# Optimization experiments

Hardware: AMD Instinct MI355X
Metric: run time of the kernel (lower is better)

The kernel has to match this reference:

```python
import jax, jax.numpy as jnp
import numpy as np

N_NODES = 50000
N_EDGES = 800000


def _gcn_norm(edge_index, n_nodes):
    # add self loops, compute symmetric normalization coefficients (PyG GCNConv)
    loop = jnp.arange(n_nodes, dtype=edge_index.dtype)
    src = jnp.concatenate([edge_index[0], loop])
    dst = jnp.concatenate([edge_index[1], loop])
    deg = jax.ops.segment_sum(jnp.ones_like(dst, dtype=jnp.float32), dst, num_segments=n_nodes)
    dinv = jnp.where(deg > 0, jax.lax.rsqrt(deg), 0.0)
    coef = dinv[src] * dinv[dst]  # [E + N]
    return src, dst, coef


def _gcn_conv(x, src, dst, coef, W, b, n_nodes):
    h = x @ W                                   # [N, out]
    msg = h[src] * coef[:, None]                # gather + scale
    agg = jax.ops.segment_sum(msg, dst, num_segments=n_nodes)
    return agg + b


def setup_inputs() -> dict:
    key = jax.random.key(0)
    ks = jax.random.split(key, 10)
    d_in, d_hid, d_out = 128, 512, 256
    num_class = [30, 25, 20, 3000]
    inp = {
        "x": jax.random.normal(ks[0], (N_NODES, d_in), dtype=jnp.float32),
        "edge_index": jax.random.randint(ks[1], (2, N_EDGES), 0, N_NODES, dtype=jnp.int64),
        "W1": jax.random.normal(ks[2], (d_in, d_hid), dtype=jnp.float32) / np.sqrt(d_in),
        "b1": jnp.zeros((d_hid,), dtype=jnp.float32),
        "W2": jax.random.normal(ks[3], (d_hid, d_out), dtype=jnp.float32) / np.sqrt(d_hid),
        "b2": jnp.zeros((d_out,), dtype=jnp.float32),
        "Wt": jax.random.normal(ks[4], (d_out, num_class[0]), dtype=jnp.float32) / np.sqrt(d_out),
        "bt": jnp.zeros((num_class[0],), dtype=jnp.float32),
        "Ws": jax.random.normal(ks[5], (d_out, num_class[1]), dtype=jnp.float32) / np.sqrt(d_out),
        "bs": jnp.zeros((num_class[1],), dtype=jnp.float32),
        "Wf": jax.random.normal(ks[6], (d_out, num_class[2]), dtype=jnp.float32) / np.sqrt(d_out),
        "bf": jnp.zeros((num_class[2],), dtype=jnp.float32),
        "Wa": jax.random.normal(ks[7], (d_out, num_class[3]), dtype=jnp.float32) / np.sqrt(d_out),
        "ba": jnp.zeros((num_class[3],), dtype=jnp.float32),
    }
    return inp


def reference(x, edge_index, W1, b1, W2, b2, Wt, bt, Ws, bs, Wf, bf, Wa, ba):
    n = x.shape[0]
    src, dst, coef = _gcn_norm(edge_index, n)
    h = jax.nn.relu(_gcn_conv(x, src, dst, coef, W1, b1, n))
    # dropout is identity at eval time
    g = _gcn_conv(h, src, dst, coef, W2, b2, n)  # graph embedding [N, 256]
    out_type = g @ Wt + bt
    out_school = g @ Ws + bs
    out_time = g @ Wf + bf
    out_author = g @ Wa + ba
    return (out_type, out_school, out_time, out_author)
```

## Files before the change

kernel.cpp:

```cpp
#include <hip/hip_runtime.h>

#define N_NODES 50000
#define N_EDGES 800000

typedef __attribute__((ext_vector_type(8))) short short8;
typedef __attribute__((ext_vector_type(4))) float f32x4;
typedef __attribute__((ext_vector_type(4))) unsigned short u16x4;

__device__ inline unsigned short f2b(float f) {
  union { float f; unsigned int u; } c; c.f = f;
  unsigned int u = c.u;
  u += 0x7FFF + ((u >> 16) & 1);
  return (unsigned short)(u >> 16);
}
__device__ inline float b2f_lo(unsigned int u) {
  union { unsigned int u; float f; } c; c.u = u << 16; return c.f;
}
__device__ inline float b2f_hi(unsigned int u) {
  union { unsigned int u; float f; } c; c.u = u & 0xFFFF0000u; return c.f;
}


__global__ void k_deg(const int* __restrict__ ei, int* __restrict__ deg) {
  int e = blockIdx.x * 256 + threadIdx.x;
  if (e < N_EDGES) atomicAdd(&deg[ei[N_EDGES + e]], 1);
}

__global__ void k_scan(const int* __restrict__ cnt, int* __restrict__ rowptr,
                       float* __restrict__ dinv) {
  __shared__ int wsum[16];
  int tid = threadIdx.x, lane = tid & 63, wv = tid >> 6;
  int carry = 0;
  for (int base = 0; base < N_NODES; base += 1024) {
    int i = base + tid;
    int v = (i < N_NODES) ? cnt[i] : 0;
    if (i < N_NODES) dinv[i] = rsqrtf((float)(v + 1));
    int s = v;
#pragma unroll
    for (int off = 1; off < 64; off <<= 1) {
      int u = __shfl_up(s, off, 64);
      if (lane >= off) s += u;
    }
    if (lane == 63) wsum[wv] = s;
    __syncthreads();
    int ws = (lane < 16) ? wsum[lane] : 0;
#pragma unroll
    for (int off = 1; off < 16; off <<= 1) {
      int u = __shfl_up(ws, off, 64);
      if (lane >= off && lane < 16) ws += u;
    }
    int wOff = (wv == 0) ? 0 : __shfl(ws, wv - 1, 64);
    int total = __shfl(ws, 15, 64);
    if (i < N_NODES) rowptr[i] = carry + wOff + (s - v);
    carry += total;
    __syncthreads();
  }
  if (tid == 0) rowptr[N_NODES] = carry;
}

__global__ void k_fill(const int* __restrict__ ei, const int* __restrict__ rowptr,
                       int* __restrict__ cur, int* __restrict__ csr) {
  int e = blockIdx.x * 256 + threadIdx.x;
  if (e < N_EDGES) {
    int d = ei[N_EDGES + e];
    int p = atomicAdd(&cur[d], 1);
    csr[rowptr[d] + p] = ei[e];
  }
}


#define CVT_UNITS (N_NODES * 128 / 4)
#define PW1_UNITS (4 * 4 * 512)
#define PW2_UNITS (2 * 16 * 512)
#define PH_UNITS  102400

__global__ void k_prep(const float* __restrict__ x, unsigned short* __restrict__ xb,
                       const float* __restrict__ W1, unsigned short* __restrict__ Bp0,
                       const float* __restrict__ W2, unsigned short* __restrict__ Bp1,
                       const float* __restrict__ Wt, const float* __restrict__ Ws,
                       const float* __restrict__ Wf, const float* __restrict__ Wa,
                       const float* __restrict__ bt, const float* __restrict__ bs,
                       const float* __restrict__ bfv, const float* __restrict__ ba,
                       unsigned short* __restrict__ BpH, float* __restrict__ bcat) {
  int idx = blockIdx.x * 256 + threadIdx.x;
  if (idx < CVT_UNITS) {
    float4 v = ((const float4*)x)[idx];
    ushort4 o; o.x = f2b(v.x); o.y = f2b(v.y); o.z = f2b(v.z); o.w = f2b(v.w);
    ((ushort4*)xb)[idx] = o;
    return;
  }
  idx -= CVT_UNITS;
  if (idx < PW1_UNITS) {
    const int KS = 4, N = 512;
    int grp = idx & 3, col = (idx >> 2) & 127;
    int rest = idx >> 9;
    int s = rest % KS, chunk = rest / KS;
    int gcol = chunk * 128 + col, k0 = s * 32 + grp * 8;
    unsigned short o[8];
#pragma unroll
    for (int j = 0; j < 8; ++j) o[j] = f2b(W1[(size_t)(k0 + j) * N + gcol]);
    *(short8*)(Bp0 + (size_t)idx * 8) = *(short8*)o;
    return;
  }
  idx -= PW1_UNITS;
  if (idx < PW2_UNITS) {
    const int KS = 16, N = 256;
    int grp = idx & 3, col = (idx >> 2) & 127;
    int rest = idx >> 9;
    int s = rest % KS, chunk = rest / KS;
    int gcol = chunk * 128 + col, k0 = s * 32 + grp * 8;
    unsigned short o[8];
#pragma unroll
    for (int j = 0; j < 8; ++j) o[j] = f2b(W2[(size_t)(k0 + j) * N + gcol]);
    *(short8*)(Bp1 + (size_t)idx * 8) = *(short8*)o;
    return;
  }
  idx -= PW2_UNITS;
  if (idx < PH_UNITS) {
    const int KS = 8;
    int grp = idx & 3, col = (idx >> 2) & 127;
    int rest = idx >> 9;
    int s = rest % KS, chunk = rest / KS;
    int gcol = chunk * 128 + col, k0 = s * 32 + grp * 8;
    const float* W = Wt; int ld = 30, c = 0;
    bool ok = true;
    if (gcol < 30)                        { W = Wt; ld = 30;   c = gcol; }
    else if (gcol < 55)                   { W = Ws; ld = 25;   c = gcol - 30; }
    else if (gcol < 75)                   { W = Wf; ld = 20;   c = gcol - 55; }
    else if (gcol >= 76 && gcol < 3076)   { W = Wa; ld = 3000; c = gcol - 76; }
    else                                  { ok = false; }
    unsigned short o[8];
#pragma unroll
    for (int j = 0; j < 8; ++j)
      o[j] = ok ? f2b(W[(size_t)(k0 + j) * ld + c]) : 0;
    *(short8*)(BpH + (size_t)idx * 8) = *(short8*)o;
    if (idx < 3200) {
      float v = 0.f;
      if (idx < 30)                      v = bt[idx];
      else if (idx < 55)                 v = bs[idx - 30];
      else if (idx < 75)                 v = bfv[idx - 55];
      else if (idx >= 76 && idx < 3076)  v = ba[idx - 76];
      bcat[idx] = v;
    }
  }
}


__global__ void k_agg1(const unsigned short* __restrict__ xb, const float* __restrict__ dinv,
                       const int* __restrict__ rowptr, const int* __restrict__ csr,
                       unsigned short* __restrict__ A1) {
  int n = blockIdx.x * 4 + (threadIdx.x >> 6);
  if (n >= N_NODES) return;
  int l = threadIdx.x & 63;
  float dn = dinv[n];
  const unsigned int* x2 = (const unsigned int*)xb;
  unsigned int sv = x2[(size_t)n * 64 + l];
  float a0 = b2f_lo(sv) * dn * dn, a1 = b2f_hi(sv) * dn * dn;
  int e = rowptr[n], e1 = rowptr[n + 1];
  for (; e + 8 <= e1; e += 8) {
    int si[8]; float cf[8]; unsigned int v[8];
#pragma unroll
    for (int j = 0; j < 8; ++j) si[j] = csr[e + j];
#pragma unroll
    for (int j = 0; j < 8; ++j) cf[j] = dinv[si[j]] * dn;
#pragma unroll
    for (int j = 0; j < 8; ++j) v[j] = x2[(size_t)si[j] * 64 + l];
#pragma unroll
    for (int j = 0; j < 8; ++j) { a0 += b2f_lo(v[j]) * cf[j]; a1 += b2f_hi(v[j]) * cf[j]; }
  }
  for (; e + 4 <= e1; e += 4) {
    int s0 = csr[e], s1 = csr[e + 1], s2 = csr[e + 2], s3 = csr[e + 3];
    float c0 = dinv[s0] * dn, c1 = dinv[s1] * dn, c2 = dinv[s2] * dn, c3 = dinv[s3] * dn;
    unsigned int v0 = x2[(size_t)s0 * 64 + l];
    unsigned int v1 = x2[(size_t)s1 * 64 + l];
    unsigned int v2 = x2[(size_t)s2 * 64 + l];
    unsigned int v3 = x2[(size_t)s3 * 64 + l];
    a0 += b2f_lo(v0) * c0 + b2f_lo(v1) * c1 + b2f_lo(v2) * c2 + b2f_lo(v3) * c3;
    a1 += b2f_hi(v0) * c0 + b2f_hi(v1) * c1 + b2f_hi(v2) * c2 + b2f_hi(v3) * c3;
  }
  for (; e < e1; ++e) {
    int s = csr[e];
    float c = dinv[s] * dn;
    unsigned int v = x2[(size_t)s * 64 + l];
    a0 += b2f_lo(v) * c; a1 += b2f_hi(v) * c;
  }
  unsigned int pk = (unsigned int)f2b(a0) | ((unsigned int)f2b(a1) << 16);
  ((unsigned int*)A1)[(size_t)n * 64 + l] = pk;
}

__global__ void k_agg2(const unsigned short* __restrict__ t, const float* __restrict__ dinv,
                       const int* __restrict__ rowptr, const int* __restrict__ csr,
                       const float* __restrict__ b2, unsigned short* __restrict__ g) {
  int n = blockIdx.x * 4 + (threadIdx.x >> 6);
  if (n >= N_NODES) return;
  int l = threadIdx.x & 63;
  float dn = dinv[n];
  const uint2* t4 = (const uint2*)t;
  uint2 sv = t4[(size_t)n * 64 + l];
  float a0 = b2f_lo(sv.x) * dn * dn, a1 = b2f_hi(sv.x) * dn * dn;
  float a2 = b2f_lo(sv.y) * dn * dn, a3 = b2f_hi(sv.y) * dn * dn;
  int e = rowptr[n], e1 = rowptr[n + 1];
  for (; e + 8 <= e1; e += 8) {
    int si[8]; float cf[8]; uint2 v[8];
#pragma unroll
    for (int j = 0; j < 8; ++j) si[j] = csr[e + j];
#pragma unroll
    for (int j = 0; j < 8; ++j) cf[j] = dinv[si[j]] * dn;
#pragma unroll
    for (int j = 0; j < 8; ++j) v[j] = t4[(size_t)si[j] * 64 + l];
#pragma unroll
    for (int j = 0; j < 8; ++j) {
      a0 += b2f_lo(v[j].x) * cf[j]; a1 += b2f_hi(v[j].x) * cf[j];
      a2 += b2f_lo(v[j].y) * cf[j]; a3 += b2f_hi(v[j].y) * cf[j];
    }
  }
  for (; e + 4 <= e1; e += 4) {
    int s0 = csr[e], s1 = csr[e + 1], s2 = csr[e + 2], s3 = csr[e + 3];
    float c0 = dinv[s0] * dn, c1 = dinv[s1] * dn, c2 = dinv[s2] * dn, c3 = dinv[s3] * dn;
    uint2 v0 = t4[(size_t)s0 * 64 + l];
    uint2 v1 = t4[(size_t)s1 * 64 + l];
    uint2 v2 = t4[(size_t)s2 * 64 + l];
    uint2 v3 = t4[(size_t)s3 * 64 + l];
    a0 += b2f_lo(v0.x) * c0 + b2f_lo(v1.x) * c1 + b2f_lo(v2.x) * c2 + b2f_lo(v3.x) * c3;
    a1 += b2f_hi(v0.x) * c0 + b2f_hi(v1.x) * c1 + b2f_hi(v2.x) * c2 + b2f_hi(v3.x) * c3;
    a2 += b2f_lo(v0.y) * c0 + b2f_lo(v1.y) * c1 + b2f_lo(v2.y) * c2 + b2f_lo(v3.y) * c3;
    a3 += b2f_hi(v0.y) * c0 + b2f_hi(v1.y) * c1 + b2f_hi(v2.y) * c2 + b2f_hi(v3.y) * c3;
  }
  for (; e < e1; ++e) {
    int s = csr[e];
    float c = dinv[s] * dn;
    uint2 v = t4[(size_t)s * 64 + l];
    a0 += b2f_lo(v.x) * c; a1 += b2f_hi(v.x) * c;
    a2 += b2f_lo(v.y) * c; a3 += b2f_hi(v.y) * c;
  }
  int d0 = l * 4;
  a0 += b2[d0]; a1 += b2[d0 + 1]; a2 += b2[d0 + 2]; a3 += b2[d0 + 3];
  ushort4 o; o.x = f2b(a0); o.y = f2b(a1); o.z = f2b(a2); o.w = f2b(a3);
  ((ushort4*)g)[(size_t)n * 64 + l] = o;
}


template <int KSTEPS, int NCHUNKS, int EPI>
__global__ __launch_bounds__(256)
void gemm_c(const unsigned short* __restrict__ A, const unsigned short* __restrict__ Bp,
            const float* __restrict__ bias, void* __restrict__ out, int M, int npanels) {
  __shared__ float lt[64][132];
  const int K = KSTEPS * 32;
  int nwg = npanels * NCHUNKS;
  int orig = blockIdx.x;
  int q = nwg >> 3, r = nwg & 7, xcd = orig & 7;
  int l = (xcd < r ? xcd * (q + 1) : r * (q + 1) + (xcd - r) * q) + (orig >> 3);
  int panel = l / NCHUNKS, chunk = l - panel * NCHUNKS;
  int tid = threadIdx.x, lane = tid & 63, w = tid >> 6;
  int ln = lane & 15, grp = lane >> 4;
  int row0 = panel * 64;

  int arow[4];
#pragma unroll
  for (int m = 0; m < 4; ++m) {
    int gr = row0 + m * 16 + ln;
    arow[m] = gr < M ? gr : M - 1;
  }

  f32x4 acc[4][2];
  f32x4 z = {0.f, 0.f, 0.f, 0.f};
#pragma unroll
  for (int m = 0; m < 4; ++m) { acc[m][0] = z; acc[m][1] = z; }

#pragma unroll 4
  for (int s = 0; s < KSTEPS; ++s) {
    short8 bfr[2];
#pragma unroll
    for (int n = 0; n < 2; ++n) {
      size_t unit = ((size_t)(chunk * KSTEPS + s) * 128 + (w * 32 + n * 16 + ln)) * 4 + grp;
      bfr[n] = *(const short8*)(Bp + unit * 8);
    }
    short8 am[4];
#pragma unroll
    for (int m = 0; m < 4; ++m)
      am[m] = *(const short8*)(A + (size_t)arow[m] * K + s * 32 + grp * 8);
#pragma unroll
    for (int m = 0; m < 4; ++m)
#pragma unroll
      for (int n = 0; n < 2; ++n)
        acc[m][n] = __builtin_amdgcn_mfma_f32_16x16x32_bf16(am[m], bfr[n], acc[m][n], 0, 0, 0);
  }

  int c0 = chunk * 128;
#pragma unroll
  for (int n = 0; n < 2; ++n) {
    int gcn = c0 + w * 32 + n * 16 + ln;
    float bv = (EPI == 1) ? 0.f : bias[gcn];
#pragma unroll
    for (int m = 0; m < 4; ++m)
#pragma unroll
      for (int rr = 0; rr < 4; ++rr) {
        float v = acc[m][n][rr] + bv;
        if (EPI == 0) v = v > 0.f ? v : 0.f;
        lt[m * 16 + grp * 4 + rr][w * 32 + n * 16 + ln] = v;
      }
  }
  __syncthreads();

  int col4 = tid & 31, rowi = tid >> 5;
#pragma unroll
  for (int rr = 0; rr < 8; ++rr) {
    int rw = rr * 8 + rowi;
    int grow = row0 + rw;
    if (grow >= M) continue;
    f32x4 v = *(const f32x4*)&lt[rw][col4 * 4];
    if (EPI == 2) {
      int gcn0 = c0 + col4 * 4;
      float* o = (float*)out;
      if (gcn0 >= 76 && gcn0 + 4 <= 3076) {
        __builtin_nontemporal_store(v, (f32x4*)(o + 3750000ull + (size_t)grow * 3000 + (gcn0 - 76)));
      } else {
#pragma unroll
        for (int j = 0; j < 4; ++j) {
          int gcn = gcn0 + j;
          if (gcn >= 3076) continue;
          size_t offo;
          if (gcn < 30)      offo = (size_t)grow * 30 + gcn;
          else if (gcn < 55) offo = 1500000ull + (size_t)grow * 25 + (gcn - 30);
          else if (gcn < 75) offo = 2750000ull + (size_t)grow * 20 + (gcn - 55);
          else if (gcn == 75) continue;
          else               offo = 3750000ull + (size_t)grow * 3000 + (gcn - 76);
          o[offo] = v[j];
        }
      }
    } else {
      const int NOUT = NCHUNKS * 128;
      u16x4 b;
      b[0] = f2b(v[0]); b[1] = f2b(v[1]); b[2] = f2b(v[2]); b[3] = f2b(v[3]);
      *(u16x4*)((unsigned short*)out + (size_t)grow * NOUT + c0 + col4 * 4) = b;
    }
  }
}


extern "C" void kernel_launch(void* const* d_in, const int* in_sizes, int n_in,
                              void* d_out, int out_size, void* d_ws, size_t ws_size,
                              hipStream_t stream) {
  const float* x  = (const float*)d_in[0];
  const int* ei   = (const int*)d_in[1];
  const float* W1 = (const float*)d_in[2];
  const float* b1 = (const float*)d_in[3];
  const float* W2 = (const float*)d_in[4];
  const float* b2 = (const float*)d_in[5];
  const float* Wt = (const float*)d_in[6];
  const float* bt = (const float*)d_in[7];
  const float* Ws = (const float*)d_in[8];
  const float* bs = (const float*)d_in[9];
  const float* Wf = (const float*)d_in[10];
  const float* bf_ = (const float*)d_in[11];
  const float* Wa = (const float*)d_in[12];
  const float* ba = (const float*)d_in[13];

  char* ws = (char*)d_ws;
  size_t off = 0;
  auto alloc = [&](size_t bytes) {
    void* p = ws + off;
    off = (off + bytes + 255) & ~(size_t)255;
    return p;
  };
  int* deg    = (int*)alloc(N_NODES * 4);
  int* cur    = (int*)alloc(N_NODES * 4);
  float* dinv = (float*)alloc(N_NODES * 4);
  int* rowptr = (int*)alloc((N_NODES + 1) * 4);
  int* csr    = (int*)alloc((size_t)N_EDGES * 4);
  unsigned short* xb = (unsigned short*)alloc((size_t)N_NODES * 128 * 2);
  unsigned short* A1 = (unsigned short*)alloc((size_t)N_NODES * 128 * 2);
  unsigned short* h  = (unsigned short*)alloc((size_t)N_NODES * 512 * 2);
  unsigned short* t  = (unsigned short*)alloc((size_t)N_NODES * 256 * 2);
  unsigned short* g  = h;
  unsigned short* Bp0 = (unsigned short*)alloc((size_t)512 * 128 * 2);
  unsigned short* Bp1 = (unsigned short*)alloc((size_t)256 * 512 * 2);
  unsigned short* BpH = (unsigned short*)alloc((size_t)3200 * 256 * 2);
  float* bcat = (float*)alloc(3200 * 4);

  const int NP = (N_NODES + 63) / 64;
  const int PREP_UNITS = CVT_UNITS + PW1_UNITS + PW2_UNITS + PH_UNITS;

  hipMemsetAsync(deg, 0, N_NODES * 4, stream);
  hipMemsetAsync(cur, 0, N_NODES * 4, stream);
  k_deg<<<(N_EDGES + 255) / 256, 256, 0, stream>>>(ei, deg);
  k_scan<<<1, 1024, 0, stream>>>(deg, rowptr, dinv);
  k_fill<<<(N_EDGES + 255) / 256, 256, 0, stream>>>(ei, rowptr, cur, csr);
  k_prep<<<(PREP_UNITS + 255) / 256, 256, 0, stream>>>(x, xb, W1, Bp0, W2, Bp1,
      Wt, Ws, Wf, Wa, bt, bs, bf_, ba, BpH, bcat);
  k_agg1<<<(N_NODES + 3) / 4, 256, 0, stream>>>(xb, dinv, rowptr, csr, A1);
  gemm_c<4, 4, 0><<<NP * 4, 256, 0, stream>>>(A1, Bp0, b1, h, N_NODES, NP);
  gemm_c<16, 2, 1><<<NP * 2, 256, 0, stream>>>(h, Bp1, nullptr, t, N_NODES, NP);
  k_agg2<<<(N_NODES + 3) / 4, 256, 0, stream>>>(t, dinv, rowptr, csr, b2, g);
  gemm_c<8, 25, 2><<<NP * 25, 256, 0, stream>>>(g, BpH, bcat, d_out, N_NODES, NP);
}
```

Baseline: 715.0 us.

## Fuse first two GEMMs through LDS and pair head GEMM column chunks

Fuses the layer-1 GEMM (with bias+ReLU) and the W2 GEMM into one kernel per 64-row panel. The 64x512 hidden tile stays in shared memory as bf16, so the N×512 intermediate is never written to or read back from global memory. The head GEMM now computes two 128-column chunks per workgroup, which reuses the A-tile loads and halves the block count. It also drops the 4-wide remainder loops in the aggregation kernels. The costs are about 66KB of LDS per block, which limits occupancy, more accumulator registers, and only NP blocks for the fused GEMM.

```diff
diff --git a/kernel.cpp b/kernel.cpp
--- a/kernel.cpp
+++ b/kernel.cpp
@@ -168,16 +168,6 @@
 #pragma unroll
     for (int j = 0; j < 8; ++j) { a0 += b2f_lo(v[j]) * cf[j]; a1 += b2f_hi(v[j]) * cf[j]; }
   }
-  for (; e + 4 <= e1; e += 4) {
-    int s0 = csr[e], s1 = csr[e + 1], s2 = csr[e + 2], s3 = csr[e + 3];
-    float c0 = dinv[s0] * dn, c1 = dinv[s1] * dn, c2 = dinv[s2] * dn, c3 = dinv[s3] * dn;
-    unsigned int v0 = x2[(size_t)s0 * 64 + l];
-    unsigned int v1 = x2[(size_t)s1 * 64 + l];
-    unsigned int v2 = x2[(size_t)s2 * 64 + l];
-    unsigned int v3 = x2[(size_t)s3 * 64 + l];
-    a0 += b2f_lo(v0) * c0 + b2f_lo(v1) * c1 + b2f_lo(v2) * c2 + b2f_lo(v3) * c3;
-    a1 += b2f_hi(v0) * c0 + b2f_hi(v1) * c1 + b2f_hi(v2) * c2 + b2f_hi(v3) * c3;
-  }
   for (; e < e1; ++e) {
     int s = csr[e];
     float c = dinv[s] * dn;
@@ -214,18 +204,6 @@
       a2 += b2f_lo(v[j].y) * cf[j]; a3 += b2f_hi(v[j].y) * cf[j];
     }
   }
-  for (; e + 4 <= e1; e += 4) {
-    int s0 = csr[e], s1 = csr[e + 1], s2 = csr[e + 2], s3 = csr[e + 3];
-    float c0 = dinv[s0] * dn, c1 = dinv[s1] * dn, c2 = dinv[s2] * dn, c3 = dinv[s3] * dn;
-    uint2 v0 = t4[(size_t)s0 * 64 + l];
-    uint2 v1 = t4[(size_t)s1 * 64 + l];
-    uint2 v2 = t4[(size_t)s2 * 64 + l];
-    uint2 v3 = t4[(size_t)s3 * 64 + l];
-    a0 += b2f_lo(v0.x) * c0 + b2f_lo(v1.x) * c1 + b2f_lo(v2.x) * c2 + b2f_lo(v3.x) * c3;
-    a1 += b2f_hi(v0.x) * c0 + b2f_hi(v1.x) * c1 + b2f_hi(v2.x) * c2 + b2f_hi(v3.x) * c3;
-    a2 += b2f_lo(v0.y) * c0 + b2f_lo(v1.y) * c1 + b2f_lo(v2.y) * c2 + b2f_lo(v3.y) * c3;
-    a3 += b2f_hi(v0.y) * c0 + b2f_hi(v1.y) * c1 + b2f_hi(v2.y) * c2 + b2f_hi(v3.y) * c3;
-  }
   for (; e < e1; ++e) {
     int s = csr[e];
     float c = dinv[s] * dn;
@@ -240,20 +218,141 @@
 }
 
 
-template <int KSTEPS, int NCHUNKS, int EPI>
 __global__ __launch_bounds__(256)
-void gemm_c(const unsigned short* __restrict__ A, const unsigned short* __restrict__ Bp,
-            const float* __restrict__ bias, void* __restrict__ out, int M, int npanels) {
-  __shared__ float lt[64][132];
-  const int K = KSTEPS * 32;
-  int nwg = npanels * NCHUNKS;
+void gemm12(const unsigned short* __restrict__ A1, const unsigned short* __restrict__ Bp0,
+            const unsigned short* __restrict__ Bp1, const float* __restrict__ b1,
+            unsigned short* __restrict__ t, int M) {
+  __shared__ char smem[66048];
+  unsigned short* hs = (unsigned short*)smem;
+  float (*lt)[132] = (float(*)[132])smem;
+  int tid = threadIdx.x, lane = tid & 63, w = tid >> 6;
+  int ln = lane & 15, grp = lane >> 4;
+  int row0 = blockIdx.x * 64;
+
+  int arow[4];
+#pragma unroll
+  for (int m = 0; m < 4; ++m) {
+    int gr = row0 + m * 16 + ln;
+    arow[m] = gr < M ? gr : M - 1;
+  }
+
+#pragma unroll 1
+  for (int c = 0; c < 4; ++c) {
+    f32x4 acc[4][2];
+    f32x4 z = {0.f, 0.f, 0.f, 0.f};
+#pragma unroll
+    for (int m = 0; m < 4; ++m) { acc[m][0] = z; acc[m][1] = z; }
+#pragma unroll
+    for (int s = 0; s < 4; ++s) {
+      short8 bfr[2];
+#pragma unroll
+      for (int n = 0; n < 2; ++n) {
+        size_t unit = ((size_t)(c * 4 + s) * 128 + (w * 32 + n * 16 + ln)) * 4 + grp;
+        bfr[n] = *(const short8*)(Bp0 + unit * 8);
+      }
+      short8 am[4];
+#pragma unroll
+      for (int m = 0; m < 4; ++m)
+        am[m] = *(const short8*)(A1 + (size_t)arow[m] * 128 + s * 32 + grp * 8);
+#pragma unroll
+      for (int m = 0; m < 4; ++m)
+#pragma unroll
+        for (int n = 0; n < 2; ++n)
+          acc[m][n] = __builtin_amdgcn_mfma_f32_16x16x32_bf16(am[m], bfr[n], acc[m][n], 0, 0, 0);
+    }
+#pragma unroll
+    for (int n = 0; n < 2; ++n) {
+      int gcn = c * 128 + w * 32 + n * 16 + ln;
+      float bv = b1[gcn];
+#pragma unroll
+      for (int m = 0; m < 4; ++m)
+#pragma unroll
+        for (int rr = 0; rr < 4; ++rr) {
+          float v = acc[m][n][rr] + bv;
+          v = v > 0.f ? v : 0.f;
+          hs[(m * 16 + grp * 4 + rr) * 516 + gcn] = f2b(v);
+        }
+    }
+  }
+  __syncthreads();
+
+  f32x4 acc2[2][4][2];
+  {
+    f32x4 z = {0.f, 0.f, 0.f, 0.f};
+#pragma unroll
+    for (int c2 = 0; c2 < 2; ++c2)
+#pragma unroll
+      for (int m = 0; m < 4; ++m) { acc2[c2][m][0] = z; acc2[c2][m][1] = z; }
+  }
+#pragma unroll 1
+  for (int c2 = 0; c2 < 2; ++c2) {
+#pragma unroll 4
+    for (int s = 0; s < 16; ++s) {
+      short8 bfr[2];
+#pragma unroll
+      for (int n = 0; n < 2; ++n) {
+        size_t unit = ((size_t)(c2 * 16 + s) * 128 + (w * 32 + n * 16 + ln)) * 4 + grp;
+        bfr[n] = *(const short8*)(Bp1 + unit * 8);
+      }
+      short8 am[4];
+#pragma unroll
+      for (int m = 0; m < 4; ++m)
+        am[m] = *(const short8*)(hs + (m * 16 + ln) * 516 + s * 32 + grp * 8);
+#pragma unroll
+      for (int m = 0; m < 4; ++m)
+#pragma unroll
+        for (int n = 0; n < 2; ++n)
+          acc2[c2][m][n] = __builtin_amdgcn_mfma_f32_16x16x32_bf16(am[m], bfr[n], acc2[c2][m][n], 0, 0, 0);
+    }
+  }
+  __syncthreads();
+
+#pragma unroll 1
+  for (int c2 = 0; c2 < 2; ++c2) {
+    int c0 = c2 * 128;
+#pragma unroll
+    for (int half = 0; half < 2; ++half) {
+      __syncthreads();
+#pragma unroll
+      for (int n = 0; n < 2; ++n)
+#pragma unroll
+        for (int mm = 0; mm < 2; ++mm) {
+          int m = half * 2 + mm;
+#pragma unroll
+          for (int rr = 0; rr < 4; ++rr)
+            lt[mm * 16 + grp * 4 + rr][w * 32 + n * 16 + ln] = acc2[c2][m][n][rr];
+        }
+      __syncthreads();
+      int col4 = tid & 31, rowi = tid >> 5;
+#pragma unroll
+      for (int rr = 0; rr < 4; ++rr) {
+        int rw = rr * 8 + rowi;
+        int grow = row0 + half * 32 + rw;
+        if (grow >= M) continue;
+        f32x4 v = *(const f32x4*)&lt[rw][col4 * 4];
+        u16x4 b;
+        b[0] = f2b(v[0]); b[1] = f2b(v[1]); b[2] = f2b(v[2]); b[3] = f2b(v[3]);
+        *(u16x4*)(t + (size_t)grow * 256 + c0 + col4 * 4) = b;
+      }
+    }
+  }
+}
+
+
+__global__ __launch_bounds__(256)
+void gemm_h2(const unsigned short* __restrict__ g, const unsigned short* __restrict__ Bp,
+             const float* __restrict__ bias, float* __restrict__ out, int M) {
+  __shared__ float lt[32][264];
+  const int NPAIR = 13, nwg = 782 * NPAIR;
   int orig = blockIdx.x;
   int q = nwg >> 3, r = nwg & 7, xcd = orig & 7;
   int l = (xcd < r ? xcd * (q + 1) : r * (q + 1) + (xcd - r) * q) + (orig >> 3);
-  int panel = l / NCHUNKS, chunk = l - panel * NCHUNKS;
+  int pan = l / NPAIR, cp = l - pan * NPAIR;
+  int c0 = cp * 256;
+  bool full = cp < 12;
   int tid = threadIdx.x, lane = tid & 63, w = tid >> 6;
   int ln = lane & 15, grp = lane >> 4;
-  int row0 = panel * 64;
+  int row0 = pan * 64;
 
   int arow[4];
 #pragma unroll
@@ -262,58 +361,74 @@
     arow[m] = gr < M ? gr : M - 1;
   }
 
-  f32x4 acc[4][2];
-  f32x4 z = {0.f, 0.f, 0.f, 0.f};
-#pragma unroll
-  for (int m = 0; m < 4; ++m) { acc[m][0] = z; acc[m][1] = z; }
-
-#pragma unroll 4
-  for (int s = 0; s < KSTEPS; ++s) {
-    short8 bfr[2];
-#pragma unroll
-    for (int n = 0; n < 2; ++n) {
-      size_t unit = ((size_t)(chunk * KSTEPS + s) * 128 + (w * 32 + n * 16 + ln)) * 4 + grp;
-      bfr[n] = *(const short8*)(Bp + unit * 8);
-    }
-    short8 am[4];
-#pragma unroll
-    for (int m = 0; m < 4; ++m)
-      am[m] = *(const short8*)(A + (size_t)arow[m] * K + s * 32 + grp * 8);
-#pragma unroll
-    for (int m = 0; m < 4; ++m)
+  f32x4 acc[2][4][2];
+  {
+    f32x4 z = {0.f, 0.f, 0.f, 0.f};
+#pragma unroll
+    for (int cc = 0; cc < 2; ++cc)
+#pragma unroll
+      for (int m = 0; m < 4; ++m) { acc[cc][m][0] = z; acc[cc][m][1] = z; }
+  }
+
+#pragma unroll 1
+  for (int cc = 0; cc < 2; ++cc) {
+    if (cc && !full) break;
+    int chunk = cp * 2 + cc;
+#pragma unroll
+    for (int s = 0; s < 8; ++s) {
+      short8 bfr[2];
+#pragma unroll
+      for (int n = 0; n < 2; ++n) {
+        size_t unit = ((size_t)(chunk * 8 + s) * 128 + (w * 32 + n * 16 + ln)) * 4 + grp;
+        bfr[n] = *(const short8*)(Bp + unit * 8);
+      }
+      short8 am[4];
+#pragma unroll
+      for (int m = 0; m < 4; ++m)
+        am[m] = *(const short8*)(g + (size_t)arow[m] * 256 + s * 32 + grp * 8);
+#pragma unroll
+      for (int m = 0; m < 4; ++m)
+#pragma unroll
+        for (int n = 0; n < 2; ++n)
+          acc[cc][m][n] = __builtin_amdgcn_mfma_f32_16x16x32_bf16(am[m], bfr[n], acc[cc][m][n], 0, 0, 0);
+    }
+  }
+
+  float bv[2][2];
+#pragma unroll
+  for (int cc = 0; cc < 2; ++cc)
+#pragma unroll
+    for (int n = 0; n < 2; ++n)
+      bv[cc][n] = bias[c0 + cc * 128 + w * 32 + n * 16 + ln];
+
+#pragma unroll
+  for (int half = 0; half < 2; ++half) {
+    if (half) __syncthreads();
+    int ccmax = full ? 2 : 1;
+    for (int cc = 0; cc < ccmax; ++cc)
 #pragma unroll
       for (int n = 0; n < 2; ++n)
-        acc[m][n] = __builtin_amdgcn_mfma_f32_16x16x32_bf16(am[m], bfr[n], acc[m][n], 0, 0, 0);
-  }
-
-  int c0 = chunk * 128;
-#pragma unroll
-  for (int n = 0; n < 2; ++n) {
-    int gcn = c0 + w * 32 + n * 16 + ln;
-    float bv = (EPI == 1) ? 0.f : bias[gcn];
-#pragma unroll
-    for (int m = 0; m < 4; ++m)
-#pragma unroll
-      for (int rr = 0; rr < 4; ++rr) {
-        float v = acc[m][n][rr] + bv;
-        if (EPI == 0) v = v > 0.f ? v : 0.f;
-        lt[m * 16 + grp * 4 + rr][w * 32 + n * 16 + ln] = v;
-      }
-  }
-  __syncthreads();
-
-  int col4 = tid & 31, rowi = tid >> 5;
-#pragma unroll
-  for (int rr = 0; rr < 8; ++rr) {
-    int rw = rr * 8 + rowi;
-    int grow = row0 + rw;
-    if (grow >= M) continue;
-    f32x4 v = *(const f32x4*)&lt[rw][col4 * 4];
-    if (EPI == 2) {
-      int gcn0 = c0 + col4 * 4;
-      float* o = (float*)out;
+#pragma unroll
+        for (int mm = 0; mm < 2; ++mm) {
+          int m = half * 2 + mm;
+#pragma unroll
+          for (int rr = 0; rr < 4; ++rr)
+            lt[mm * 16 + grp * 4 + rr][cc * 128 + w * 32 + n * 16 + ln] =
+                acc[cc][m][n][rr] + bv[cc][n];
+        }
+    __syncthreads();
+
+    int u = tid & 63;
+#pragma unroll
+    for (int rr = 0; rr < 8; ++rr) {
+      int rw = rr * 4 + (tid >> 6);
+      int grow = row0 + half * 32 + rw;
+      if (grow >= M) continue;
+      if (!full && u >= 32) continue;
+      f32x4 v = *(const f32x4*)&lt[rw][u * 4];
+      int gcn0 = c0 + u * 4;
       if (gcn0 >= 76 && gcn0 + 4 <= 3076) {
-        __builtin_nontemporal_store(v, (f32x4*)(o + 3750000ull + (size_t)grow * 3000 + (gcn0 - 76)));
+        __builtin_nontemporal_store(v, (f32x4*)(out + 3750000ull + (size_t)grow * 3000 + (gcn0 - 76)));
       } else {
 #pragma unroll
         for (int j = 0; j < 4; ++j) {
@@ -325,14 +440,9 @@
           else if (gcn < 75) offo = 2750000ull + (size_t)grow * 20 + (gcn - 55);
           else if (gcn == 75) continue;
           else               offo = 3750000ull + (size_t)grow * 3000 + (gcn - 76);
-          o[offo] = v[j];
+          out[offo] = v[j];
         }
       }
-    } else {
-      const int NOUT = NCHUNKS * 128;
-      u16x4 b;
-      b[0] = f2b(v[0]); b[1] = f2b(v[1]); b[2] = f2b(v[2]); b[3] = f2b(v[3]);
-      *(u16x4*)((unsigned short*)out + (size_t)grow * NOUT + c0 + col4 * 4) = b;
     }
   }
 }
@@ -370,9 +480,8 @@
   int* csr    = (int*)alloc((size_t)N_EDGES * 4);
   unsigned short* xb = (unsigned short*)alloc((size_t)N_NODES * 128 * 2);
   unsigned short* A1 = (unsigned short*)alloc((size_t)N_NODES * 128 * 2);
-  unsigned short* h  = (unsigned short*)alloc((size_t)N_NODES * 512 * 2);
   unsigned short* t  = (unsigned short*)alloc((size_t)N_NODES * 256 * 2);
-  unsigned short* g  = h;
+  unsigned short* g  = (unsigned short*)alloc((size_t)N_NODES * 256 * 2);
   unsigned short* Bp0 = (unsigned short*)alloc((size_t)512 * 128 * 2);
   unsigned short* Bp1 = (unsigned short*)alloc((size_t)256 * 512 * 2);
   unsigned short* BpH = (unsigned short*)alloc((size_t)3200 * 256 * 2);
@@ -389,8 +498,7 @@
   k_prep<<<(PREP_UNITS + 255) / 256, 256, 0, stream>>>(x, xb, W1, Bp0, W2, Bp1,
       Wt, Ws, Wf, Wa, bt, bs, bf_, ba, BpH, bcat);
   k_agg1<<<(N_NODES + 3) / 4, 256, 0, stream>>>(xb, dinv, rowptr, csr, A1);
-  gemm_c<4, 4, 0><<<NP * 4, 256, 0, stream>>>(A1, Bp0, b1, h, N_NODES, NP);
-  gemm_c<16, 2, 1><<<NP * 2, 256, 0, stream>>>(h, Bp1, nullptr, t, N_NODES, NP);
+  gemm12<<<NP, 256, 0, stream>>>(A1, Bp0, Bp1, b1, t, N_NODES);
   k_agg2<<<(N_NODES + 3) / 4, 256, 0, stream>>>(t, dinv, rowptr, csr, b2, g);
-  gemm_c<8, 25, 2><<<NP * 25, 256, 0, stream>>>(g, BpH, bcat, d_out, N_NODES, NP);
-}
+  gemm_h2<<<NP * 13, 256, 0, stream>>>(g, BpH, bcat, (float*)d_out, N_NODES);
+}
```

After: 1.286 ms. 1.8x slower.

## Use persistent-row head GEMM looping over all column chunks per block

Applied to the files above, without the earlier changes.

Replaces the head GEMM launch, which used one block per (row panel, column chunk), with a dedicated kernel where each block owns a 64-row panel and loops over all 25 column chunks. The A rows stay hot in cache or registers across chunks, and the launch has 25x fewer blocks. The trade-off is less parallelism (about 782 blocks) and no pipelining across chunks, with an extra barrier per chunk. It also removes the 4-wide remainder loops from both aggregation kernels, which shrinks code size.

```diff
diff --git a/kernel.cpp b/kernel.cpp
--- a/kernel.cpp
+++ b/kernel.cpp
@@ -168,16 +168,6 @@
 #pragma unroll
     for (int j = 0; j < 8; ++j) { a0 += b2f_lo(v[j]) * cf[j]; a1 += b2f_hi(v[j]) * cf[j]; }
   }
-  for (; e + 4 <= e1; e += 4) {
-    int s0 = csr[e], s1 = csr[e + 1], s2 = csr[e + 2], s3 = csr[e + 3];
-    float c0 = dinv[s0] * dn, c1 = dinv[s1] * dn, c2 = dinv[s2] * dn, c3 = dinv[s3] * dn;
-    unsigned int v0 = x2[(size_t)s0 * 64 + l];
-    unsigned int v1 = x2[(size_t)s1 * 64 + l];
-    unsigned int v2 = x2[(size_t)s2 * 64 + l];
-    unsigned int v3 = x2[(size_t)s3 * 64 + l];
-    a0 += b2f_lo(v0) * c0 + b2f_lo(v1) * c1 + b2f_lo(v2) * c2 + b2f_lo(v3) * c3;
-    a1 += b2f_hi(v0) * c0 + b2f_hi(v1) * c1 + b2f_hi(v2) * c2 + b2f_hi(v3) * c3;
-  }
   for (; e < e1; ++e) {
     int s = csr[e];
     float c = dinv[s] * dn;
@@ -214,18 +204,6 @@
       a2 += b2f_lo(v[j].y) * cf[j]; a3 += b2f_hi(v[j].y) * cf[j];
     }
   }
-  for (; e + 4 <= e1; e += 4) {
-    int s0 = csr[e], s1 = csr[e + 1], s2 = csr[e + 2], s3 = csr[e + 3];
-    float c0 = dinv[s0] * dn, c1 = dinv[s1] * dn, c2 = dinv[s2] * dn, c3 = dinv[s3] * dn;
-    uint2 v0 = t4[(size_t)s0 * 64 + l];
-    uint2 v1 = t4[(size_t)s1 * 64 + l];
-    uint2 v2 = t4[(size_t)s2 * 64 + l];
-    uint2 v3 = t4[(size_t)s3 * 64 + l];
-    a0 += b2f_lo(v0.x) * c0 + b2f_lo(v1.x) * c1 + b2f_lo(v2.x) * c2 + b2f_lo(v3.x) * c3;
-    a1 += b2f_hi(v0.x) * c0 + b2f_hi(v1.x) * c1 + b2f_hi(v2.x) * c2 + b2f_hi(v3.x) * c3;
-    a2 += b2f_lo(v0.y) * c0 + b2f_lo(v1.y) * c1 + b2f_lo(v2.y) * c2 + b2f_lo(v3.y) * c3;
-    a3 += b2f_hi(v0.y) * c0 + b2f_hi(v1.y) * c1 + b2f_hi(v2.y) * c2 + b2f_hi(v3.y) * c3;
-  }
   for (; e < e1; ++e) {
     int s = csr[e];
     float c = dinv[s] * dn;
@@ -309,11 +287,84 @@
     int grow = row0 + rw;
     if (grow >= M) continue;
     f32x4 v = *(const f32x4*)&lt[rw][col4 * 4];
-    if (EPI == 2) {
+    const int NOUT = NCHUNKS * 128;
+    u16x4 b;
+    b[0] = f2b(v[0]); b[1] = f2b(v[1]); b[2] = f2b(v[2]); b[3] = f2b(v[3]);
+    *(u16x4*)((unsigned short*)out + (size_t)grow * NOUT + c0 + col4 * 4) = b;
+  }
+}
+
+
+__global__ __launch_bounds__(256)
+void gemm_hp(const unsigned short* __restrict__ A, const unsigned short* __restrict__ Bp,
+             const float* __restrict__ bias, float* __restrict__ out, int M) {
+  __shared__ float lt[64][132];
+  int tid = threadIdx.x, lane = tid & 63, w = tid >> 6;
+  int ln = lane & 15, grp = lane >> 4;
+  int row0 = blockIdx.x * 64;
+
+  int arow[4];
+#pragma unroll
+  for (int m = 0; m < 4; ++m) {
+    int gr = row0 + m * 16 + ln;
+    arow[m] = gr < M ? gr : M - 1;
+  }
+  int col4 = tid & 31, rowi = tid >> 5;
+
+#pragma unroll 1
+  for (int chunk = 0; chunk < 25; ++chunk) {
+    f32x4 acc[4][2];
+    f32x4 z = {0.f, 0.f, 0.f, 0.f};
+#pragma unroll
+    for (int m = 0; m < 4; ++m) { acc[m][0] = z; acc[m][1] = z; }
+#pragma unroll
+    for (int s = 0; s < 8; ++s) {
+      short8 bfr[2];
+#pragma unroll
+      for (int n = 0; n < 2; ++n) {
+        size_t unit = ((size_t)(chunk * 8 + s) * 128 + (w * 32 + n * 16 + ln)) * 4 + grp;
+        bfr[n] = *(const short8*)(Bp + unit * 8);
+      }
+      short8 am[4];
+#pragma unroll
+      for (int m = 0; m < 4; ++m)
+        am[m] = *(const short8*)(A + (size_t)arow[m] * 256 + s * 32 + grp * 8);
+#pragma unroll
+      for (int m = 0; m < 4; ++m)
+#pragma unroll
+        for (int n = 0; n < 2; ++n)
+          acc[m][n] = __builtin_amdgcn_mfma_f32_16x16x32_bf16(am[m], bfr[n], acc[m][n], 0, 0, 0);
+    }
+
+    int c0 = chunk * 128;
+    if (chunk) {
+      asm volatile("s_waitcnt lgkmcnt(0)" ::: "memory");
+      __builtin_amdgcn_s_barrier();
+      asm volatile("" ::: "memory");
+    }
+#pragma unroll
+    for (int n = 0; n < 2; ++n) {
+      int gcn = c0 + w * 32 + n * 16 + ln;
+      float bv = bias[gcn];
+#pragma unroll
+      for (int m = 0; m < 4; ++m)
+#pragma unroll
+        for (int rr = 0; rr < 4; ++rr)
+          lt[m * 16 + grp * 4 + rr][w * 32 + n * 16 + ln] = acc[m][n][rr] + bv;
+    }
+    asm volatile("s_waitcnt lgkmcnt(0)" ::: "memory");
+    __builtin_amdgcn_s_barrier();
+    asm volatile("" ::: "memory");
+
+#pragma unroll
+    for (int rr = 0; rr < 8; ++rr) {
+      int rw = rr * 8 + rowi;
+      int grow = row0 + rw;
+      if (grow >= M) continue;
+      f32x4 v = *(const f32x4*)&lt[rw][col4 * 4];
       int gcn0 = c0 + col4 * 4;
-      float* o = (float*)out;
       if (gcn0 >= 76 && gcn0 + 4 <= 3076) {
-        __builtin_nontemporal_store(v, (f32x4*)(o + 3750000ull + (size_t)grow * 3000 + (gcn0 - 76)));
+        __builtin_nontemporal_store(v, (f32x4*)(out + 3750000ull + (size_t)grow * 3000 + (gcn0 - 76)));
       } else {
 #pragma unroll
         for (int j = 0; j < 4; ++j) {
@@ -325,14 +376,9 @@
           else if (gcn < 75) offo = 2750000ull + (size_t)grow * 20 + (gcn - 55);
           else if (gcn == 75) continue;
           else               offo = 3750000ull + (size_t)grow * 3000 + (gcn - 76);
-          o[offo] = v[j];
+          out[offo] = v[j];
         }
       }
-    } else {
-      const int NOUT = NCHUNKS * 128;
-      u16x4 b;
-      b[0] = f2b(v[0]); b[1] = f2b(v[1]); b[2] = f2b(v[2]); b[3] = f2b(v[3]);
-      *(u16x4*)((unsigned short*)out + (size_t)grow * NOUT + c0 + col4 * 4) = b;
     }
   }
 }
@@ -392,5 +438,5 @@
   gemm_c<4, 4, 0><<<NP * 4, 256, 0, stream>>>(A1, Bp0, b1, h, N_NODES, NP);
   gemm_c<16, 2, 1><<<NP * 2, 256, 0, stream>>>(h, Bp1, nullptr, t, N_NODES, NP);
   k_agg2<<<(N_NODES + 3) / 4, 256, 0, stream>>>(t, dinv, rowptr, csr, b2, g);
-  gemm_c<8, 25, 2><<<NP * 25, 256, 0, stream>>>(g, BpH, bcat, d_out, N_NODES, NP);
-}
+  gemm_hp<<<NP, 256, 0, stream>>>(g, BpH, bcat, (float*)d_out, N_NODES);
+}
```

After: 743.5 us. +4.0%, slower.
